# Kernel optimization log

Measured on AMD Instinct MI355X. Metric: run time of the kernel, lower is better.

Reference implementation:

```python
import jax, jax.numpy as jnp
import numpy as np

K = 3  # spatial window (window_size = [1,3,3,1])


def _extract_patches(x, k):
    """TF-style extract_patches, VALID padding, stride 1, rate 1.
    x: [B,H,W,C] -> [B,Ho,Wo,k*k*C] with depth ordering (ki, kj, c)."""
    B, H, W, C = x.shape
    Ho, Wo = H - k + 1, W - k + 1
    cols = [x[:, ki:ki + Ho, kj:kj + Wo, :] for ki in range(k) for kj in range(k)]
    return jnp.concatenate(cols, axis=-1)


def setup_inputs() -> dict:
    key = jax.random.key(0)
    k1, k2 = jax.random.split(key)
    x = jax.random.normal(k1, (8, 32, 32, 32), dtype=jnp.float32)
    # weight shape per build(): (1, 1, 1, K*K*C, filters) = (1,1,1,288,64)
    w = jax.random.normal(k2, (1, 1, 1, 3 * 3 * 32, 64), dtype=jnp.float32) * 0.05
    bias = jnp.zeros((64,), dtype=jnp.float32)
    return {"x": x, "w": w, "bias": bias}


def reference(x, w, bias):
    # patches: [B,Ho,Wo,KKC]
    p = _extract_patches(x, K)
    # broadcast add: [B,Ho,Wo,KKC,1] + [KKC,F] -> [B,Ho,Wo,KKC,F]
    r = p[..., None] + w[0, 0, 0]
    # tropical conv: max-plus minus min-plus over the patch axis, plus bias
    return jnp.max(r, axis=3) - jnp.min(r, axis=3) + bias
```

## Files before the change

kernel.cpp:

```cpp
#include <hip/hip_runtime.h>
#include <math.h>


#define WSTRIDE 100

__global__ __launch_bounds__(512) void trop_kernel(
    const float* __restrict__ x, const float* __restrict__ w,
    const float* __restrict__ bias, float* __restrict__ out) {
  __shared__ float wt[64 * WSTRIDE];

  const int i = blockIdx.x;
  const int b = blockIdx.y;
  const int tid = threadIdx.x;
  const int f = tid & 63;
  const int j0 = __builtin_amdgcn_readfirstlane(tid >> 6) * 4;

  const int skq = tid >> 6;

  float mx[4] = {-INFINITY, -INFINITY, -INFINITY, -INFINITY};
  float mn[4] = {INFINITY, INFINITY, INFINITY, INFINITY};
  float bv = bias[f];

  for (int ki = 0; ki < 3; ++ki) {
    __syncthreads();
#pragma unroll
    for (int it = 0; it < 3; ++it) {
      int k0 = (it * 8 + skq) * 4;
      float4 v;
      v.x = w[(ki * 96 + k0 + 0) * 64 + f];
      v.y = w[(ki * 96 + k0 + 1) * 64 + f];
      v.z = w[(ki * 96 + k0 + 2) * 64 + f];
      v.w = w[(ki * 96 + k0 + 3) * 64 + f];
      *(float4*)(&wt[f * WSTRIDE + k0]) = v;
    }
    __syncthreads();

    const float* xr = x + (((size_t)b * 32 + (i + ki)) * 32) * 32;
    int cc[6];
#pragma unroll
    for (int col = 0; col < 6; ++col) cc[col] = (j0 + col < 32) ? j0 + col : 31;

#pragma unroll
    for (int c8 = 0; c8 < 32; c8 += 8) {
      float4 xa[6][2];
#pragma unroll
      for (int col = 0; col < 6; ++col) {
        xa[col][0] = *(const float4*)(xr + cc[col] * 32 + c8);
        xa[col][1] = *(const float4*)(xr + cc[col] * 32 + c8 + 4);
      }
      float4 wv[3][2];
#pragma unroll
      for (int kj = 0; kj < 3; ++kj) {
        const float* wrow = &wt[f * WSTRIDE + kj * 32 + c8];
        wv[kj][0] = *(const float4*)(wrow);
        wv[kj][1] = *(const float4*)(wrow + 4);
      }
#pragma unroll
      for (int c = 0; c < 8; ++c) {
        float w0 = ((const float*)&wv[0][0])[c];
        float w1 = ((const float*)&wv[1][0])[c];
        float w2 = ((const float*)&wv[2][0])[c];
#pragma unroll
        for (int p = 0; p < 4; ++p) {
          float a0 = ((const float*)&xa[p + 0][0])[c] + w0;
          float a1 = ((const float*)&xa[p + 1][0])[c] + w1;
          float a2 = ((const float*)&xa[p + 2][0])[c] + w2;
          mx[p] = fmaxf(mx[p], fmaxf(a0, fmaxf(a1, a2)));
          mn[p] = fminf(mn[p], fminf(a0, fminf(a1, a2)));
        }
      }
    }
  }

  float* ob = out + (((size_t)b * 30 + i) * 30 + j0) * 64 + f;
#pragma unroll
  for (int p = 0; p < 4; ++p)
    if (j0 + p < 30) ob[(size_t)p * 64] = mx[p] - mn[p] + bv;
}

extern "C" void kernel_launch(void* const* d_in, const int* in_sizes, int n_in,
                              void* d_out, int out_size, void* d_ws, size_t ws_size,
                              hipStream_t stream) {
  const float* x = (const float*)d_in[0];
  const float* w = (const float*)d_in[1];
  const float* bias = (const float*)d_in[2];
  float* out = (float*)d_out;
  dim3 grid(30, 8);
  dim3 block(512);
  hipLaunchKernelGGL(trop_kernel, grid, block, 0, stream, x, w, bias, out);
}
```

Before: 68.43 us.

## Convert weights and input rows to fp16 in LDS and use packed half2 max/min

Stages all 288x64 weights and the three input rows in shared memory as fp16 once per block, replacing the per-ki weight reloads and direct global float4 reads of x. The inner loop then uses packed half2 add/max/min, handling two channels per instruction, and reduces the two lanes at the end. This aims to halve ALU instruction count and cut LDS and global traffic. The cost is reduced precision: fp16 rounding of inputs and weights plus fp16 accumulation of max-min, which may exceed the tolerance.

```diff
diff --git a/kernel.cpp b/kernel.cpp
--- a/kernel.cpp
+++ b/kernel.cpp
@@ -2,12 +2,16 @@
 #include <math.h>
 
 
-#define WSTRIDE 100
+typedef _Float16 half2v __attribute__((ext_vector_type(2)));
+typedef _Float16 half8v __attribute__((ext_vector_type(8)));
+
+#define WSTRIDE 296
 
 __global__ __launch_bounds__(512) void trop_kernel(
     const float* __restrict__ x, const float* __restrict__ w,
     const float* __restrict__ bias, float* __restrict__ out) {
-  __shared__ float wt[64 * WSTRIDE];
+  __shared__ _Float16 wt[64 * WSTRIDE];
+  __shared__ _Float16 xh[3 * 32 * 32];
 
   const int i = blockIdx.x;
   const int b = blockIdx.y;
@@ -16,66 +20,87 @@
   const int j0 = __builtin_amdgcn_readfirstlane(tid >> 6) * 4;
 
   const int skq = tid >> 6;
+#pragma unroll
+  for (int it = 0; it < 9; ++it) {
+    int k0 = (it * 8 + skq) * 4;
+    const float* wp = w + (size_t)k0 * 64 + f;
+    _Float16 h0 = (_Float16)wp[0 * 64];
+    _Float16 h1 = (_Float16)wp[1 * 64];
+    _Float16 h2 = (_Float16)wp[2 * 64];
+    _Float16 h3 = (_Float16)wp[3 * 64];
+    half2v* dst = (half2v*)&wt[f * WSTRIDE + k0];
+    dst[0] = half2v{h0, h1};
+    dst[1] = half2v{h2, h3};
+  }
 
-  float mx[4] = {-INFINITY, -INFINITY, -INFINITY, -INFINITY};
-  float mn[4] = {INFINITY, INFINITY, INFINITY, INFINITY};
-  float bv = bias[f];
+  const float* xb = x + (((size_t)b * 32 + i) * 32) * 32;
+#pragma unroll
+  for (int t = 0; t < 3; ++t) {
+    int g = tid + t * 512;
+    int ki = g >> 9;
+    int rem = g & 511;
+    int col = rem >> 4;
+    int cp = rem & 15;
+    float2 v = *(const float2*)(xb + ki * 1024 + col * 32 + cp * 2);
+    *(half2v*)&xh[(ki * 32 + col) * 32 + cp * 2] =
+        half2v{(_Float16)v.x, (_Float16)v.y};
+  }
 
-  for (int ki = 0; ki < 3; ++ki) {
-    __syncthreads();
+  __syncthreads();
+
+  half2v mxp[4], mnp[4];
+  const _Float16 NI = (_Float16)(-INFINITY), PI = (_Float16)INFINITY;
 #pragma unroll
-    for (int it = 0; it < 3; ++it) {
-      int k0 = (it * 8 + skq) * 4;
-      float4 v;
-      v.x = w[(ki * 96 + k0 + 0) * 64 + f];
-      v.y = w[(ki * 96 + k0 + 1) * 64 + f];
-      v.z = w[(ki * 96 + k0 + 2) * 64 + f];
-      v.w = w[(ki * 96 + k0 + 3) * 64 + f];
-      *(float4*)(&wt[f * WSTRIDE + k0]) = v;
-    }
-    __syncthreads();
-
-    const float* xr = x + (((size_t)b * 32 + (i + ki)) * 32) * 32;
-    int cc[6];
-#pragma unroll
-    for (int col = 0; col < 6; ++col) cc[col] = (j0 + col < 32) ? j0 + col : 31;
+  for (int p = 0; p < 4; ++p) {
+    mxp[p] = half2v{NI, NI};
+    mnp[p] = half2v{PI, PI};
+  }
 
 #pragma unroll
+  for (int ki = 0; ki < 3; ++ki) {
+#pragma unroll
     for (int c8 = 0; c8 < 32; c8 += 8) {
-      float4 xa[6][2];
+      half2v xv[6][4];
 #pragma unroll
       for (int col = 0; col < 6; ++col) {
-        xa[col][0] = *(const float4*)(xr + cc[col] * 32 + c8);
-        xa[col][1] = *(const float4*)(xr + cc[col] * 32 + c8 + 4);
+        int cc = (j0 + col < 32) ? j0 + col : 31;
+        half8v hv = *(const half8v*)&xh[(ki * 32 + cc) * 32 + c8];
+#pragma unroll
+        for (int q = 0; q < 4; ++q) xv[col][q] = half2v{hv[2 * q], hv[2 * q + 1]};
       }
-      float4 wv[3][2];
+      half2v wv[3][4];
 #pragma unroll
       for (int kj = 0; kj < 3; ++kj) {
-        const float* wrow = &wt[f * WSTRIDE + kj * 32 + c8];
-        wv[kj][0] = *(const float4*)(wrow);
-        wv[kj][1] = *(const float4*)(wrow + 4);
+        half8v hv = *(const half8v*)&wt[f * WSTRIDE + ki * 96 + kj * 32 + c8];
+#pragma unroll
+        for (int q = 0; q < 4; ++q) wv[kj][q] = half2v{hv[2 * q], hv[2 * q + 1]};
       }
 #pragma unroll
-      for (int c = 0; c < 8; ++c) {
-        float w0 = ((const float*)&wv[0][0])[c];
-        float w1 = ((const float*)&wv[1][0])[c];
-        float w2 = ((const float*)&wv[2][0])[c];
+      for (int q = 0; q < 4; ++q) {
 #pragma unroll
-        for (int p = 0; p < 4; ++p) {
-          float a0 = ((const float*)&xa[p + 0][0])[c] + w0;
-          float a1 = ((const float*)&xa[p + 1][0])[c] + w1;
-          float a2 = ((const float*)&xa[p + 2][0])[c] + w2;
-          mx[p] = fmaxf(mx[p], fmaxf(a0, fmaxf(a1, a2)));
-          mn[p] = fminf(mn[p], fminf(a0, fminf(a1, a2)));
+        for (int kj = 0; kj < 3; ++kj) {
+          half2v wq = wv[kj][q];
+#pragma unroll
+          for (int p = 0; p < 4; ++p) {
+            half2v a = xv[p + kj][q] + wq;
+            mxp[p] = __builtin_elementwise_max(mxp[p], a);
+            mnp[p] = __builtin_elementwise_min(mnp[p], a);
+          }
         }
       }
     }
   }
 
+  float bv = bias[f];
   float* ob = out + (((size_t)b * 30 + i) * 30 + j0) * 64 + f;
 #pragma unroll
-  for (int p = 0; p < 4; ++p)
-    if (j0 + p < 30) ob[(size_t)p * 64] = mx[p] - mn[p] + bv;
+  for (int p = 0; p < 4; ++p) {
+    if (j0 + p < 30) {
+      float m = fmaxf((float)mxp[p].x, (float)mxp[p].y);
+      float n = fminf((float)mnp[p].x, (float)mnp[p].y);
+      ob[(size_t)p * 64] = m - n + bv;
+    }
+  }
 }
 
 extern "C" void kernel_launch(void* const* d_in, const int* in_sizes, int n_in,
```

Result: slower. 93.44 us (+36.5%).
